# Kernel optimization log

Hardware: AMD Instinct MI355X
Metric: run time of the kernel (lower is better)

The kernel has to match this reference:

```python
import jax, jax.numpy as jnp
import numpy as np

N_NODES = 25000
N_EDGES = 400000
MUL0 = 16      # multiplicity of 0e
MUL1 = 8       # multiplicity of 1o
H = 64         # radial MLP width (= dist_embedding dim)
WEIGHT_NUMEL = MUL0*MUL0 + MUL0*MUL1 + MUL1*MUL1 + MUL1*MUL0  # 576
NUM_NEIGHBORS = 16
INV_SQRT3 = 0.57735026918962576  # w3j normalization for l=1 paths
PW0 = (1.0/24.0)**0.5  # path weight, 0e out: alpha = dim(0e)/ (16+8)
PW1 = (3.0/24.0)**0.5  # path weight, 1o out: alpha = dim(1o)/ (16+8)
SILU_NORM = 1.6791767923989418  # e3nn normalize2mom factor for silu


def _radial_mlp(d, W1, W2):
    # e3nn FullyConnectedNet([H, H, WEIGHT_NUMEL], silu): x @ W / sqrt(fan_in),
    # activation normalized to unit second moment.
    h = SILU_NORM * jax.nn.silu(d @ W1 / jnp.sqrt(jnp.asarray(H, d.dtype)))
    return h @ W2 / jnp.sqrt(jnp.asarray(H, d.dtype))


def _tensor_product(x, y, w):
    # x: [E, 40] gathered node feats; y: [E, 4] edge_attr; w: [E, 576]
    x0 = x[:, :MUL0]                        # [E,16]  0e
    x1 = x[:, MUL0:].reshape(-1, MUL1, 3)   # [E,8,3] 1o
    y0 = y[:, :1]                           # [E,1]   0e
    y1 = y[:, 1:4]                          # [E,3]   1o
    s = MUL0*MUL0
    w1 = w[:, :s].reshape(-1, MUL0, MUL0)                       # 0e*0e->0e
    w2 = w[:, s:s+MUL0*MUL1].reshape(-1, MUL0, MUL1)            # 0e*1o->1o
    s2 = s + MUL0*MUL1
    w3 = w[:, s2:s2+MUL1*MUL1].reshape(-1, MUL1, MUL1)          # 1o*0e->1o
    s3 = s2 + MUL1*MUL1
    w4 = w[:, s3:].reshape(-1, MUL1, MUL0)                      # 1o*1o->0e
    out0 = PW0 * (jnp.einsum('eu,euw->ew', x0 * y0, w1)
                  + INV_SQRT3 * jnp.einsum('eui,ei,euw->ew', x1, y1, w4))
    out1 = PW1 * INV_SQRT3 * (jnp.einsum('eu,ej,euw->ewj', x0, y1, w2)
                              + jnp.einsum('eui,euw->ewi', x1 * y0[:, :, None], w3))
    return jnp.concatenate([out0, out1.reshape(-1, MUL1*3)], axis=1)  # [E,40]


def setup_inputs() -> dict:
    key = jax.random.key(0)
    ks = jax.random.split(key, 7)
    node_input = jax.random.normal(ks[0], (N_NODES, MUL0 + 3*MUL1), jnp.float32)
    edge_src = jax.random.randint(ks[1], (N_EDGES,), 0, N_NODES)
    edge_dst = jax.random.randint(ks[2], (N_EDGES,), 0, N_NODES)
    edge_attr = jax.random.normal(ks[3], (N_EDGES, 4), jnp.float32)
    dist_embedding = jax.random.normal(ks[4], (N_EDGES, H), jnp.float32)
    W1 = jax.random.normal(ks[5], (H, H), jnp.float32)
    W2 = jax.random.normal(ks[6], (H, WEIGHT_NUMEL), jnp.float32)
    return {"node_input": node_input, "edge_src": edge_src, "edge_dst": edge_dst,
            "edge_attr": edge_attr, "dist_embedding": dist_embedding,
            "W1": W1, "W2": W2}


def reference(node_input, edge_src, edge_dst, edge_attr, dist_embedding, W1, W2):
    tp_weights = _radial_mlp(dist_embedding, W1, W2)            # [E,576]
    edge_features = _tensor_product(node_input[edge_dst], edge_attr, tp_weights)
    node_features = jax.ops.segment_sum(edge_features, edge_src,
                                        num_segments=N_NODES)
    return node_features / jnp.sqrt(jnp.asarray(NUM_NEIGHBORS, node_features.dtype))
```

## Files before the change

### kernel.cpp

```cpp
#include <hip/hip_runtime.h>

#define N_NODES 25000
#define N_EDGES 400000

static constexpr float INV_SQRT3 = 0.5773502691896257f;
static constexpr float PW0 = 0.20412414523193154f;
static constexpr float PW1 = 0.35355339059327373f;
static constexpr float SILU_NORM = 1.6791767923989418f;
static constexpr float SCC = 0.03125f;
static constexpr float KP1C = PW1 * INV_SQRT3 * SCC;
static constexpr float Q4C  = PW0 * INV_SQRT3 * SCC;

typedef __attribute__((ext_vector_type(8))) short bf16x8;
typedef __attribute__((ext_vector_type(4))) float f32x4;

#define XQS 60

__device__ __forceinline__ unsigned short f2bf(float x) {
    unsigned int u = __float_as_uint(x);
    u += 0x7FFFu + ((u >> 16) & 1u);
    return (unsigned short)(u >> 16);
}

__device__ __forceinline__ bf16x8 pack8(const float* p) {
    float4 a = *(const float4*)p, b = *(const float4*)(p + 4);
    bf16x8 r;
    r[0] = (short)f2bf(a.x); r[1] = (short)f2bf(a.y);
    r[2] = (short)f2bf(a.z); r[3] = (short)f2bf(a.w);
    r[4] = (short)f2bf(b.x); r[5] = (short)f2bf(b.y);
    r[6] = (short)f2bf(b.z); r[7] = (short)f2bf(b.w);
    return r;
}

#define WS_CNT  0
#define WS_CUR  25000
#define WS_EIDX 50000
#define WS_W1T  450000
#define WS_W2T  452048
#define WS_REQ_BYTES ((size_t)(452048 + 18432) * 4)

__global__ __launch_bounds__(256) void k_preph(const int* __restrict__ edge_src,
                                               int* __restrict__ cnt,
                                               const float* __restrict__ W1,
                                               const float* __restrict__ W2,
                                               unsigned short* __restrict__ W1Tg,
                                               unsigned short* __restrict__ W2Tg)
{
    const int id = blockIdx.x * 256 + threadIdx.x;
    if (id < N_EDGES) atomicAdd(&cnt[edge_src[id]], 1);
    if (id < 64 * 64) {
        const int n = id >> 6, j = id & 63;
        W1Tg[n * 64 + j] = f2bf(W1[j * 64 + n]);
    }
    if (id < 576 * 64) {
        const int n = id / 64, k = id % 64;
        W2Tg[n * 64 + k] = f2bf(W2[k * 576 + n]);
    }
}

__global__ __launch_bounds__(1024) void k_scan(const int* __restrict__ cnt,
                                               int* __restrict__ cur)
{
    __shared__ int sa[1024], sb[1024];
    const int t = threadIdx.x;
    const int base = t * 25;
    int loc[25];
    int s = 0;
#pragma unroll
    for (int q = 0; q < 25; ++q) {
        const int idx = base + q;
        const int v = (idx < N_NODES) ? cnt[idx] : 0;
        loc[q] = s; s += v;
    }
    sa[t] = s;
    __syncthreads();
    int* sp = sa; int* dp = sb;
    for (int d = 1; d < 1024; d <<= 1) {
        int v = sp[t];
        if (t >= d) v += sp[t - d];
        dp[t] = v;
        __syncthreads();
        int* tmp = sp; sp = dp; dp = tmp;
    }
    const int excl = sp[t] - s;
#pragma unroll
    for (int q = 0; q < 25; ++q) {
        const int idx = base + q;
        if (idx < N_NODES) cur[idx] = excl + loc[q];
    }
}

__global__ __launch_bounds__(256) void k_scatter(const int* __restrict__ edge_src,
                                                 int* __restrict__ cur,
                                                 int* __restrict__ eidx)
{
    const int e = blockIdx.x * 256 + threadIdx.x;
    if (e < N_EDGES) {
        const int pos = atomicAdd(&cur[edge_src[e]], 1);
        eidx[pos] = e;
    }
}

__global__ __launch_bounds__(256, 4) void k_conv(
    const float* __restrict__ node_input,
    const int* __restrict__ edge_src,
    const int* __restrict__ edge_dst,
    const float* __restrict__ edge_attr,
    const float* __restrict__ dist_embedding,
    const unsigned short* __restrict__ W1Tg,
    const unsigned short* __restrict__ W2Tg,
    const int* __restrict__ eidx_g,
    float* __restrict__ out)
{
    __shared__ __align__(16) unsigned short sH[64 * 64];
    __shared__ float xq_s[64 * XQS];
    __shared__ float racc[64 * 40];
    __shared__ int   eidx_s[64], src_s[64], p0_s[64];

    const int t  = threadIdx.x;
    const int pb = blockIdx.x * 64;
    const int w = t >> 6, lane = t & 63;
    const int kgrp = lane >> 4;
    const int cl = lane & 15;

    if (t < 64) {
        const int eid = eidx_g[pb + t];
        eidx_s[t] = eid;
        src_s[t]  = edge_src[eid];
        const int dst = edge_dst[eid];
        const float4* xr = (const float4*)(node_input + (size_t)dst * 40);
        float* xd = xq_s + t * XQS;
        float xx[40];
#pragma unroll
        for (int i = 0; i < 10; ++i) {
            float4 v = xr[i];
            xx[i*4+0] = v.x; xx[i*4+1] = v.y; xx[i*4+2] = v.z; xx[i*4+3] = v.w;
            *(float4*)(xd + i * 4) = v;
        }
        const float4 yv = *(const float4*)(edge_attr + (size_t)eid * 4);
        xd[48] = PW0 * SCC * yv.x;
        xd[49] = KP1C * yv.x;
        xd[50] = yv.y; xd[51] = yv.z; xd[52] = yv.w;
#pragma unroll
        for (int u = 0; u < 8; ++u)
            xd[40 + u] = yv.y * xx[16 + u*3] + yv.z * xx[16 + u*3 + 1] + yv.w * xx[16 + u*3 + 2];
    }
    for (int i = t; i < 64 * 40; i += 256) racc[i] = 0.f;
    __syncthreads();

    {
        const int er = w * 16 + cl;
        const float* dp = dist_embedding + (size_t)eidx_s[er] * 64 + kgrp * 8;
        bf16x8 a0 = pack8(dp);
        bf16x8 a1 = pack8(dp + 32);
        bf16x8 wb0[4], wb1[4];
#pragma unroll
        for (int nt = 0; nt < 4; ++nt) {
            const unsigned short* bp = W1Tg + (nt * 16 + cl) * 64 + kgrp * 8;
            wb0[nt] = *(const bf16x8*)bp;
            wb1[nt] = *(const bf16x8*)(bp + 32);
        }
#pragma unroll
        for (int nt = 0; nt < 4; ++nt) {
            f32x4 c = {0.f, 0.f, 0.f, 0.f};
            c = __builtin_amdgcn_mfma_f32_16x16x32_bf16(a0, wb0[nt], c, 0, 0, 0);
            c = __builtin_amdgcn_mfma_f32_16x16x32_bf16(a1, wb1[nt], c, 0, 0, 0);
#pragma unroll
            for (int r = 0; r < 4; ++r) {
                const float zz = 0.125f * c[r];
                const float h = SILU_NORM * __fdividef(zz, 1.f + __expf(-zz));
                const int hr = w * 16 + kgrp * 4 + r;
                const int hc = nt * 16 + cl;
                sH[hr * 64 + (hc ^ ((hr & 7) << 3))] = f2bf(h);
            }
        }
    }
    if (t < 64) {
        int p = t;
        while (p > 0 && src_s[p - 1] == src_s[t]) --p;
        p0_s[t] = p;
    }
    __syncthreads();

    const int arow = w * 16 + cl;
    const unsigned short* ap = sH + arow * 64;
    const int ax = (cl & 7) << 3;
    bf16x8 A0 = *(const bf16x8*)(ap + ((kgrp * 8) ^ ax));
    bf16x8 A1 = *(const bf16x8*)(ap + ((32 + kgrp * 8) ^ ax));

    float r1a[4] = {0,0,0,0}, r4a[4] = {0,0,0,0}, Tt[4] = {0,0,0,0};
    float P0[4] = {0,0,0,0}, P1[4] = {0,0,0,0}, P2[4] = {0,0,0,0};
    const int e0 = w * 16 + kgrp * 4;
    const unsigned short* bbase = W2Tg + cl * 64 + kgrp * 8;

    bf16x8 Rb0[4], Rb1[4];
#pragma unroll
    for (int i = 0; i < 3; ++i) {
        const unsigned short* bp = bbase + i * 1024;
        Rb0[i] = *(const bf16x8*)bp;
        Rb1[i] = *(const bf16x8*)(bp + 32);
    }
#pragma unroll
    for (int gnt = 0; gnt < 36; ++gnt) {
        if (gnt < 33) {
            const unsigned short* bp = bbase + (gnt + 3) * 1024;
            Rb0[(gnt + 3) & 3] = *(const bf16x8*)bp;
            Rb1[(gnt + 3) & 3] = *(const bf16x8*)(bp + 32);
        }
        f32x4 c = {0.f, 0.f, 0.f, 0.f};
        c = __builtin_amdgcn_mfma_f32_16x16x32_bf16(A0, Rb0[gnt & 3], c, 0, 0, 0);
        c = __builtin_amdgcn_mfma_f32_16x16x32_bf16(A1, Rb1[gnt & 3], c, 0, 0, 0);
        if (gnt < 16) {
#pragma unroll
            for (int r = 0; r < 4; ++r) r1a[r] += xq_s[(e0 + r) * XQS + gnt] * c[r];
        } else if (gnt < 24) {
            const int u = (gnt - 16) * 2 + ((lane >> 3) & 1);
#pragma unroll
            for (int r = 0; r < 4; ++r) Tt[r] += xq_s[(e0 + r) * XQS + u] * c[r];
        } else if (gnt < 28) {
            const int u = (gnt - 24) * 2 + ((lane >> 3) & 1);
#pragma unroll
            for (int r = 0; r < 4; ++r) {
                const float* xp = xq_s + (e0 + r) * XQS + 16 + u * 3;
                P0[r] += xp[0] * c[r];
                P1[r] += xp[1] * c[r];
                P2[r] += xp[2] * c[r];
            }
        } else {
            const int u = gnt - 28;
#pragma unroll
            for (int r = 0; r < 4; ++r) r1a[r] = r1a[r], r4a[r] += xq_s[(e0 + r) * XQS + 40 + u] * c[r];
        }
    }

#pragma unroll
    for (int r = 0; r < 4; ++r) {
        const int e = e0 + r;
        const float v = xq_s[e * XQS + 48] * r1a[r] + Q4C * r4a[r];
        atomicAdd(&racc[p0_s[e] * 40 + cl], v);
    }
#pragma unroll
    for (int r = 0; r < 4; ++r) {
        Tt[r] += __shfl_xor(Tt[r], 8);
        P0[r] += __shfl_xor(P0[r], 8);
        P1[r] += __shfl_xor(P1[r], 8);
        P2[r] += __shfl_xor(P2[r], 8);
    }
    if ((lane & 8) == 0) {
        const int wo = lane & 7;
#pragma unroll
        for (int r = 0; r < 4; ++r) {
            const int e = e0 + r;
            const float q3  = xq_s[e * XQS + 49];
            const float y1x = xq_s[e * XQS + 50];
            const float y1y = xq_s[e * XQS + 51];
            const float y1z = xq_s[e * XQS + 52];
            float* rp = &racc[p0_s[e] * 40 + 16 + wo * 3];
            atomicAdd(rp + 0, KP1C * y1x * Tt[r] + q3 * P0[r]);
            atomicAdd(rp + 1, KP1C * y1y * Tt[r] + q3 * P1[r]);
            atomicAdd(rp + 2, KP1C * y1z * Tt[r] + q3 * P2[r]);
        }
    }
    __syncthreads();
    if (t < 64 && p0_s[t] == t) {
        float* op = out + (size_t)src_s[t] * 40;
        const float* rp = racc + t * 40;
#pragma unroll
        for (int cc = 0; cc < 40; ++cc) atomicAdd(op + cc, rp[cc]);
    }
}

template <int NC>
__device__ __forceinline__ void gemm_cols(const float* __restrict__ base,
                                          const float (&h)[64], float (&w)[NC]) {
#pragma unroll
    for (int i = 0; i < NC; ++i) w[i] = 0.f;
#pragma unroll
    for (int k = 0; k < 64; ++k) {
        const float4* r4 = (const float4*)(base + k * 576);
        const float hk = h[k];
#pragma unroll
        for (int q = 0; q < NC / 4; ++q) {
            float4 a = r4[q];
            w[q * 4 + 0] += hk * a.x;  w[q * 4 + 1] += hk * a.y;
            w[q * 4 + 2] += hk * a.z;  w[q * 4 + 3] += hk * a.w;
        }
    }
}

__global__ __launch_bounds__(256) void conv_atomic(
    const float* __restrict__ node_input,
    const int* __restrict__ edge_src,
    const int* __restrict__ edge_dst,
    const float* __restrict__ edge_attr,
    const float* __restrict__ dist_embedding,
    const float* __restrict__ W1,
    const float* __restrict__ W2,
    float* __restrict__ out)
{
    __shared__ float sX[256 * 44];
    const int e = blockIdx.x * 256 + threadIdx.x;
    if (e >= N_EDGES) return;
    float* xs = &sX[threadIdx.x * 44];

    float z[64];
#pragma unroll
    for (int k = 0; k < 64; ++k) z[k] = 0.f;
    const float4* dp = (const float4*)(dist_embedding + (size_t)e * 64);
#pragma unroll 2
    for (int j4 = 0; j4 < 16; ++j4) {
        float4 d4 = dp[j4];
        float dj[4] = {d4.x, d4.y, d4.z, d4.w};
#pragma unroll
        for (int r = 0; r < 4; ++r) {
            const float4* w1r = (const float4*)(W1 + (j4 * 4 + r) * 64);
            const float dv = dj[r];
#pragma unroll
            for (int k4 = 0; k4 < 16; ++k4) {
                float4 a = w1r[k4];
                z[k4 * 4 + 0] += dv * a.x; z[k4 * 4 + 1] += dv * a.y;
                z[k4 * 4 + 2] += dv * a.z; z[k4 * 4 + 3] += dv * a.w;
            }
        }
    }
    float h[64];
#pragma unroll
    for (int k = 0; k < 64; ++k) {
        const float zz = 0.125f * z[k];
        h[k] = SILU_NORM * __fdividef(zz, 1.f + __expf(-zz));
    }
    const int dst = edge_dst[e];
    const float4* xr = (const float4*)(node_input + (size_t)dst * 40);
    float4* xd = (float4*)xs;
#pragma unroll
    for (int i = 0; i < 10; ++i) xd[i] = xr[i];
    const float4 yv = *(const float4*)(edge_attr + (size_t)e * 4);
    const float q0 = PW0 * yv.x * SCC;
    const float q4 = PW0 * INV_SQRT3 * SCC;
    const float q20 = KP1C * yv.y, q21 = KP1C * yv.z, q22 = KP1C * yv.w;
    const float q3 = KP1C * yv.x;
    float o0[16], o1[24];
#pragma unroll
    for (int i = 0; i < 16; ++i) o0[i] = 0.f;
#pragma unroll
    for (int i = 0; i < 24; ++i) o1[i] = 0.f;
#pragma unroll 1
    for (int u = 0; u < 16; ++u) {
        float w[16];
        gemm_cols<16>(W2 + u * 16, h, w);
        const float coef = q0 * xs[u];
#pragma unroll
        for (int i = 0; i < 16; ++i) o0[i] += coef * w[i];
    }
#pragma unroll 1
    for (int u = 0; u < 16; ++u) {
        float w[8];
        gemm_cols<8>(W2 + 256 + u * 8, h, w);
        const float xv = xs[u];
        const float c0 = q20 * xv, c1 = q21 * xv, c2 = q22 * xv;
#pragma unroll
        for (int i = 0; i < 8; ++i) {
            o1[i * 3 + 0] += c0 * w[i]; o1[i * 3 + 1] += c1 * w[i]; o1[i * 3 + 2] += c2 * w[i];
        }
    }
#pragma unroll 1
    for (int u = 0; u < 8; ++u) {
        float w[8];
        gemm_cols<8>(W2 + 384 + u * 8, h, w);
        const float c0 = q3 * xs[16 + u * 3 + 0];
        const float c1 = q3 * xs[16 + u * 3 + 1];
        const float c2 = q3 * xs[16 + u * 3 + 2];
#pragma unroll
        for (int i = 0; i < 8; ++i) {
            o1[i * 3 + 0] += c0 * w[i]; o1[i * 3 + 1] += c1 * w[i]; o1[i * 3 + 2] += c2 * w[i];
        }
    }
#pragma unroll 1
    for (int u = 0; u < 8; ++u) {
        float w[16];
        gemm_cols<16>(W2 + 448 + u * 16, h, w);
        const float b = q4 * (xs[16 + u * 3 + 0] * yv.y +
                              xs[16 + u * 3 + 1] * yv.z +
                              xs[16 + u * 3 + 2] * yv.w);
#pragma unroll
        for (int i = 0; i < 16; ++i) o0[i] += b * w[i];
    }
    const int src = edge_src[e];
    float* op = out + (size_t)src * 40;
#pragma unroll
    for (int i = 0; i < 16; ++i) atomicAdd(op + i, o0[i]);
#pragma unroll
    for (int i = 0; i < 24; ++i) atomicAdd(op + 16 + i, o1[i]);
}

extern "C" void kernel_launch(void* const* d_in, const int* in_sizes, int n_in,
                              void* d_out, int out_size, void* d_ws, size_t ws_size,
                              hipStream_t stream)
{
    const float* node_input     = (const float*)d_in[0];
    const int*   edge_src       = (const int*)d_in[1];
    const int*   edge_dst       = (const int*)d_in[2];
    const float* edge_attr      = (const float*)d_in[3];
    const float* dist_embedding = (const float*)d_in[4];
    const float* W1             = (const float*)d_in[5];
    const float* W2             = (const float*)d_in[6];
    float* out = (float*)d_out;

    hipMemsetAsync(out, 0, (size_t)out_size * sizeof(float), stream);

    if (ws_size < WS_REQ_BYTES || d_ws == nullptr) {
        dim3 grid((N_EDGES + 255) / 256);
        conv_atomic<<<grid, 256, 0, stream>>>(node_input, edge_src, edge_dst,
                                              edge_attr, dist_embedding, W1, W2, out);
        return;
    }

    int* wsI = (int*)d_ws;
    int* cnt  = wsI + WS_CNT;
    int* cur  = wsI + WS_CUR;
    int* eidx = wsI + WS_EIDX;
    unsigned short* W1Tg = (unsigned short*)(wsI + WS_W1T);
    unsigned short* W2Tg = (unsigned short*)(wsI + WS_W2T);

    hipMemsetAsync(cnt, 0, (size_t)N_NODES * sizeof(int), stream);
    k_preph<<<dim3((N_EDGES + 255) / 256), 256, 0, stream>>>(edge_src, cnt,
                                                             W1, W2, W1Tg, W2Tg);
    k_scan<<<dim3(1), 1024, 0, stream>>>(cnt, cur);
    k_scatter<<<dim3((N_EDGES + 255) / 256), 256, 0, stream>>>(edge_src, cur, eidx);
    k_conv<<<dim3(N_EDGES / 64), 256, 0, stream>>>(node_input, edge_src, edge_dst,
                                                   edge_attr, dist_embedding,
                                                   W1Tg, W2Tg, eidx, out);
}
```

Before: 465.8 us.

## Stage W2 weights through swizzled LDS in chunks and prefetch dist embedding early

The W2 bf16 weight matrix is now XOR-swizzled at prep time. It is staged cooperatively into a 96x64 LDS buffer in six chunks, with register double-buffering of the next chunk. This replaces each wave loading its B fragments directly from global memory. The dist_embedding row loads are hoisted to kernel entry so their latency overlaps the node gather. Launch bounds drop the min-blocks hint. The cost is 12KB more LDS and extra block-wide barriers per chunk, which may reduce occupancy.

```diff
diff --git a/kernel.cpp b/kernel.cpp
--- a/kernel.cpp
+++ b/kernel.cpp
@@ -22,8 +22,7 @@
     return (unsigned short)(u >> 16);
 }
 
-__device__ __forceinline__ bf16x8 pack8(const float* p) {
-    float4 a = *(const float4*)p, b = *(const float4*)(p + 4);
+__device__ __forceinline__ bf16x8 pack2(float4 a, float4 b) {
     bf16x8 r;
     r[0] = (short)f2bf(a.x); r[1] = (short)f2bf(a.y);
     r[2] = (short)f2bf(a.z); r[3] = (short)f2bf(a.w);
@@ -54,7 +53,7 @@
     }
     if (id < 576 * 64) {
         const int n = id / 64, k = id % 64;
-        W2Tg[n * 64 + k] = f2bf(W2[k * 576 + n]);
+        W2Tg[n * 64 + (k ^ ((n & 7) << 3))] = f2bf(W2[k * 576 + n]);
     }
 }
 
@@ -101,7 +100,7 @@
     }
 }
 
-__global__ __launch_bounds__(256, 4) void k_conv(
+__global__ __launch_bounds__(256) void k_conv(
     const float* __restrict__ node_input,
     const int* __restrict__ edge_src,
     const int* __restrict__ edge_dst,
@@ -112,21 +111,36 @@
     const int* __restrict__ eidx_g,
     float* __restrict__ out)
 {
+    __shared__ __align__(16) unsigned short sB[96 * 64];
     __shared__ __align__(16) unsigned short sH[64 * 64];
     __shared__ float xq_s[64 * XQS];
     __shared__ float racc[64 * 40];
-    __shared__ int   eidx_s[64], src_s[64], p0_s[64];
+    __shared__ int   src_s[64], p0_s[64];
 
     const int t  = threadIdx.x;
     const int pb = blockIdx.x * 64;
     const int w = t >> 6, lane = t & 63;
     const int kgrp = lane >> 4;
     const int cl = lane & 15;
+    const int bx = (cl & 7) << 3;
+
+    const int er = w * 16 + cl;
+    const int eidA = eidx_g[pb + er];
+    const float* dpp = dist_embedding + (size_t)eidA * 64 + kgrp * 8;
+    float4 d0a = *(const float4*)dpp;
+    float4 d0b = *(const float4*)(dpp + 4);
+    float4 d1a = *(const float4*)(dpp + 32);
+    float4 d1b = *(const float4*)(dpp + 36);
+
+    const uint4* W2v = (const uint4*)W2Tg;
+    uint4* sBv = (uint4*)sB;
+    uint4 st0 = W2v[t];
+    uint4 st1 = W2v[t + 256];
+    uint4 st2 = W2v[t + 512];
 
     if (t < 64) {
         const int eid = eidx_g[pb + t];
-        eidx_s[t] = eid;
-        src_s[t]  = edge_src[eid];
+        src_s[t] = edge_src[eid];
         const int dst = edge_dst[eid];
         const float4* xr = (const float4*)(node_input + (size_t)dst * 40);
         float* xd = xq_s + t * XQS;
@@ -149,10 +163,8 @@
     __syncthreads();
 
     {
-        const int er = w * 16 + cl;
-        const float* dp = dist_embedding + (size_t)eidx_s[er] * 64 + kgrp * 8;
-        bf16x8 a0 = pack8(dp);
-        bf16x8 a1 = pack8(dp + 32);
+        bf16x8 a0 = pack2(d0a, d0b);
+        bf16x8 a1 = pack2(d1a, d1b);
         bf16x8 wb0[4], wb1[4];
 #pragma unroll
         for (int nt = 0; nt < 4; ++nt) {
@@ -180,56 +192,61 @@
         while (p > 0 && src_s[p - 1] == src_s[t]) --p;
         p0_s[t] = p;
     }
+    sBv[t] = st0; sBv[t + 256] = st1; sBv[t + 512] = st2;
+    st0 = W2v[768 + t]; st1 = W2v[768 + t + 256]; st2 = W2v[768 + t + 512];
     __syncthreads();
 
     const int arow = w * 16 + cl;
     const unsigned short* ap = sH + arow * 64;
-    const int ax = (cl & 7) << 3;
-    bf16x8 A0 = *(const bf16x8*)(ap + ((kgrp * 8) ^ ax));
-    bf16x8 A1 = *(const bf16x8*)(ap + ((32 + kgrp * 8) ^ ax));
+    bf16x8 A0 = *(const bf16x8*)(ap + ((kgrp * 8) ^ bx));
+    bf16x8 A1 = *(const bf16x8*)(ap + ((32 + kgrp * 8) ^ bx));
 
     float r1a[4] = {0,0,0,0}, r4a[4] = {0,0,0,0}, Tt[4] = {0,0,0,0};
     float P0[4] = {0,0,0,0}, P1[4] = {0,0,0,0}, P2[4] = {0,0,0,0};
     const int e0 = w * 16 + kgrp * 4;
-    const unsigned short* bbase = W2Tg + cl * 64 + kgrp * 8;
-
-    bf16x8 Rb0[4], Rb1[4];
-#pragma unroll
-    for (int i = 0; i < 3; ++i) {
-        const unsigned short* bp = bbase + i * 1024;
-        Rb0[i] = *(const bf16x8*)bp;
-        Rb1[i] = *(const bf16x8*)(bp + 32);
-    }
-#pragma unroll
-    for (int gnt = 0; gnt < 36; ++gnt) {
-        if (gnt < 33) {
-            const unsigned short* bp = bbase + (gnt + 3) * 1024;
-            Rb0[(gnt + 3) & 3] = *(const bf16x8*)bp;
-            Rb1[(gnt + 3) & 3] = *(const bf16x8*)(bp + 32);
-        }
-        f32x4 c = {0.f, 0.f, 0.f, 0.f};
-        c = __builtin_amdgcn_mfma_f32_16x16x32_bf16(A0, Rb0[gnt & 3], c, 0, 0, 0);
-        c = __builtin_amdgcn_mfma_f32_16x16x32_bf16(A1, Rb1[gnt & 3], c, 0, 0, 0);
-        if (gnt < 16) {
-#pragma unroll
-            for (int r = 0; r < 4; ++r) r1a[r] += xq_s[(e0 + r) * XQS + gnt] * c[r];
-        } else if (gnt < 24) {
-            const int u = (gnt - 16) * 2 + ((lane >> 3) & 1);
-#pragma unroll
-            for (int r = 0; r < 4; ++r) Tt[r] += xq_s[(e0 + r) * XQS + u] * c[r];
-        } else if (gnt < 28) {
-            const int u = (gnt - 24) * 2 + ((lane >> 3) & 1);
-#pragma unroll
-            for (int r = 0; r < 4; ++r) {
-                const float* xp = xq_s + (e0 + r) * XQS + 16 + u * 3;
-                P0[r] += xp[0] * c[r];
-                P1[r] += xp[1] * c[r];
-                P2[r] += xp[2] * c[r];
+
+#pragma unroll
+    for (int p = 0; p < 6; ++p) {
+        if (p > 0) {
+            __syncthreads();
+            sBv[t] = st0; sBv[t + 256] = st1; sBv[t + 512] = st2;
+            if (p < 5) {
+                st0 = W2v[(p + 1) * 768 + t];
+                st1 = W2v[(p + 1) * 768 + t + 256];
+                st2 = W2v[(p + 1) * 768 + t + 512];
             }
-        } else {
-            const int u = gnt - 28;
-#pragma unroll
-            for (int r = 0; r < 4; ++r) r1a[r] = r1a[r], r4a[r] += xq_s[(e0 + r) * XQS + 40 + u] * c[r];
+            __syncthreads();
+        }
+#pragma unroll
+        for (int nt = 0; nt < 6; ++nt) {
+            const int gnt = p * 6 + nt;
+            const unsigned short* bp = sB + (nt * 16 + cl) * 64;
+            bf16x8 B0 = *(const bf16x8*)(bp + ((kgrp * 8) ^ bx));
+            bf16x8 B1 = *(const bf16x8*)(bp + ((32 + kgrp * 8) ^ bx));
+            f32x4 c = {0.f, 0.f, 0.f, 0.f};
+            c = __builtin_amdgcn_mfma_f32_16x16x32_bf16(A0, B0, c, 0, 0, 0);
+            c = __builtin_amdgcn_mfma_f32_16x16x32_bf16(A1, B1, c, 0, 0, 0);
+            if (gnt < 16) {
+#pragma unroll
+                for (int r = 0; r < 4; ++r) r1a[r] += xq_s[(e0 + r) * XQS + gnt] * c[r];
+            } else if (gnt < 24) {
+                const int u = (gnt - 16) * 2 + ((lane >> 3) & 1);
+#pragma unroll
+                for (int r = 0; r < 4; ++r) Tt[r] += xq_s[(e0 + r) * XQS + u] * c[r];
+            } else if (gnt < 28) {
+                const int u = (gnt - 24) * 2 + ((lane >> 3) & 1);
+#pragma unroll
+                for (int r = 0; r < 4; ++r) {
+                    const float* xp = xq_s + (e0 + r) * XQS + 16 + u * 3;
+                    P0[r] += xp[0] * c[r];
+                    P1[r] += xp[1] * c[r];
+                    P2[r] += xp[2] * c[r];
+                }
+            } else {
+                const int u = gnt - 28;
+#pragma unroll
+                for (int r = 0; r < 4; ++r) r4a[r] += xq_s[(e0 + r) * XQS + 40 + u] * c[r];
+            }
         }
     }
 
```

Result: faster. 388.0 us (-16.7%).
